# Optimization experiments

Measured on AMD Instinct MI355X. Metric: run time of the kernel, lower is better.

The kernel has to match this reference:

```python
import jax, jax.numpy as jnp
import numpy as np

B, N_ROIS, C, H, W = 4, 180, 512, 48, 48
STRIDE = 4
EPS = 1e-5


def _pool_one(feat, roi):
    # feat: [C,H,W], roi: [4] float (y1,x1,y2,x2) in image coords
    r = roi / STRIDE
    r0 = jnp.trunc(r[0]).astype(jnp.int32)
    r1 = jnp.trunc(r[1]).astype(jnp.int32)
    r2 = jnp.ceil(r[2]).astype(jnp.int32)
    r3 = jnp.ceil(r[3]).astype(jnp.int32)
    h_size = r2 - r0 + 1
    w_size = r3 - r1 + 1
    idx2 = jnp.arange(2)
    # AdaptiveMaxPool2d region boundaries: [floor(i*s/2), ceil((i+1)*s/2))
    sh = (idx2 * h_size) // 2
    eh = ((idx2 + 1) * h_size + 1) // 2
    sw = (idx2 * w_size) // 2
    ew = ((idx2 + 1) * w_size + 1) // 2
    hh = jnp.arange(H)[None, :]
    ww = jnp.arange(W)[None, :]
    mask_h = (hh >= (r0 + sh)[:, None]) & (hh < (r0 + eh)[:, None])  # [2,H]
    mask_w = (ww >= (r1 + sw)[:, None]) & (ww < (r1 + ew)[:, None])  # [2,W]
    neg = jnp.finfo(feat.dtype).min
    # max over W within each col region -> [2(oj), C, H]
    mw = jnp.where(mask_w[:, None, None, :], feat[None], neg).max(axis=-1)
    # max over H within each row region -> [2(oi), 2(oj), C]
    p = jnp.where(mask_h[:, None, None, :], mw[None], neg).max(axis=-1)
    # torch layout: [C, oi, oj] then flatten row-major
    return jnp.transpose(p, (2, 0, 1)).reshape(-1)  # [C*4]


def _roi_pool(features, rois):
    # features: [B,C,H,W], rois: [B,N,4] -> [B,N,C*4]
    def per_roi(roi_b):  # roi_b: [B,4]
        return jax.vmap(_pool_one)(features, roi_b)  # [B, C*4]
    out = jax.lax.map(per_roi, jnp.swapaxes(rois, 0, 1))  # [N,B,C*4]
    return jnp.swapaxes(out, 0, 1)


def _bn(x, gamma, beta):
    # training-mode BatchNorm1d over [B, N_ROIS(channels), F]: stats over (B,F)
    mean = x.mean(axis=(0, 2), keepdims=True)
    var = ((x - mean) ** 2).mean(axis=(0, 2), keepdims=True)
    return (x - mean) * jax.lax.rsqrt(var + EPS) * gamma[None, :, None] + beta[None, :, None]


def setup_inputs() -> dict:
    key = jax.random.key(0)
    k1, k2, k3, k4, k5 = jax.random.split(key, 5)
    features = jax.random.normal(k1, (B, C, H, W), dtype=jnp.float32)
    max_coord = (H - 1) * STRIDE
    y = jnp.sort(jax.random.uniform(k2, (B, N_ROIS, 2), minval=0.0, maxval=max_coord), axis=-1)
    x = jnp.sort(jax.random.uniform(k3, (B, N_ROIS, 2), minval=0.0, maxval=max_coord), axis=-1)
    rois = jnp.stack([y[..., 0], x[..., 0], y[..., 1], x[..., 1]], axis=-1)  # [B,N,4]
    F_in = C * 4
    W1 = jax.random.normal(k4, (64, F_in), dtype=jnp.float32) * 0.02
    bl1 = jnp.zeros((64,), dtype=jnp.float32)
    gamma1 = jnp.ones((N_ROIS,), dtype=jnp.float32)
    beta1 = jnp.zeros((N_ROIS,), dtype=jnp.float32)
    gamma2 = jnp.ones((N_ROIS,), dtype=jnp.float32)
    beta2 = jnp.zeros((N_ROIS,), dtype=jnp.float32)
    return {"features": features, "rois": rois, "gamma1": gamma1, "beta1": beta1,
            "W1": W1, "bl1": bl1, "gamma2": gamma2, "beta2": beta2}


def reference(features, rois, gamma1, beta1, W1, bl1, gamma2, beta2):
    pooled = _roi_pool(features, rois)            # [B, 180, 2048]
    x = jax.nn.relu(pooled)
    x = _bn(x, gamma1, beta1)
    y = jnp.einsum('bnf,of->bno', x, W1) + bl1    # [B, 180, 64]
    y = _bn(y, gamma2, beta2)
    return y
```

## Files before the change

### kernel.cpp

```cpp
#include <hip/hip_runtime.h>
#include <hip/hip_bf16.h>
#include <cfloat>
#include <math.h>

#define BB 4
#define NR 180
#define CC 512
#define HH 48
#define WW 48
#define FF (CC*4)
#define OO 64
#define EPSV 1e-5f
#define NCH 4


__device__ __forceinline__ void unpk(unsigned u, float& lo, float& hi) {
    lo = __uint_as_float(u << 16);
    hi = __uint_as_float(u & 0xffff0000u);
}
__device__ __forceinline__ unsigned pk(float lo, float hi) {
    return (__float_as_uint(lo) >> 16) | (__float_as_uint(hi) & 0xffff0000u);
}
__device__ __forceinline__ void acc8(float* cm, uint4 u) {
    float a, b;
    unpk(u.x, a, b); cm[0] = fmaxf(cm[0], a); cm[1] = fmaxf(cm[1], b);
    unpk(u.y, a, b); cm[2] = fmaxf(cm[2], a); cm[3] = fmaxf(cm[3], b);
    unpk(u.z, a, b); cm[4] = fmaxf(cm[4], a); cm[5] = fmaxf(cm[5], b);
    unpk(u.w, a, b); cm[6] = fmaxf(cm[6], a); cm[7] = fmaxf(cm[7], b);
}

__global__ __launch_bounds__(256) void k_prep(const float* __restrict__ feat,
                                              const float* __restrict__ W1,
                                              __hip_bfloat16* __restrict__ featB,
                                              float* __restrict__ W1T4) {
    __shared__ float tile[32][33];
    int t = threadIdx.x;
    int z = blockIdx.z;

    if (z < 4) {
        const int S = HH * WW;
        int b  = z;
        int s0 = blockIdx.x * 32;
        int c0 = blockIdx.y * 32;
        const float* src = feat + (size_t)b * CC * S;
        ushort* dst = (ushort*)featB + (size_t)b * S * CC;

        int cl = t >> 3;
        int sx = (t & 7) << 2;
        float4 v = *(const float4*)(src + (size_t)(c0 + cl) * S + s0 + sx);
        tile[cl][sx] = v.x; tile[cl][sx+1] = v.y; tile[cl][sx+2] = v.z; tile[cl][sx+3] = v.w;
        __syncthreads();

        int sl = t >> 3;
        int c4 = (t & 7) << 2;
        unsigned u0 = pk(tile[c4][sl],   tile[c4+1][sl]);
        unsigned u1 = pk(tile[c4+2][sl], tile[c4+3][sl]);
        *(uint2*)(dst + (size_t)(s0 + sl) * CC + c0 + c4) = make_uint2(u0, u1);
    } else {
        if (blockIdx.x >= 8) return;
        int kt = blockIdx.y * 8 + blockIdx.x;
        int k0 = (kt >> 1) * 32, o0 = (kt & 1) * 32;
        int tx = t & 31, ty = t >> 5;
        #pragma unroll
        for (int k = 0; k < 4; k++) {
            int row = ty + k * 8;
            tile[row][tx] = W1[(size_t)(o0 + row) * FF + (k0 + tx)];
        }
        __syncthreads();
        #pragma unroll
        for (int k = 0; k < 4; k++) {
            int row = ty + k * 8;
            int kk = k0 + row;
            int o  = o0 + tx;
            W1T4[(size_t)(kk >> 2) * 256 + o * 4 + (kk & 3)] = tile[tx][row];
        }
    }
}

__global__ __launch_bounds__(256, 6) void k_pool(const ushort* __restrict__ featB,
                                                 const float* __restrict__ rois,
                                                 ushort* __restrict__ pp) {
    __shared__ unsigned lu[4][16][64];
    int ch = blockIdx.x;
    int bn = blockIdx.y;
    int b = bn & 3, n = bn >> 2;
    int tid = threadIdx.x;
    int g  = tid >> 6;
    int c  = tid & 63;
    int c8 = c << 3;

    const float* roi = rois + ((size_t)b * NR + n) * 4;
    int r0 = (int)(roi[0] * 0.25f);
    int r1 = (int)(roi[1] * 0.25f);
    int r2 = (int)ceilf(roi[2] * 0.25f);
    int r3 = (int)ceilf(roi[3] * 0.25f);
    int hs  = r2 - r0 + 1;
    int wsz = r3 - r1 + 1;
    int eh0 = (hs + 1) >> 1, sh1 = hs >> 1;
    int ew0 = (wsz + 1) >> 1, sw1 = wsz >> 1;

    const float NEG = -FLT_MAX;
    float q00[8], q01[8], q10[8], q11[8];
    #pragma unroll
    for (int j = 0; j < 8; j++) { q00[j]=NEG; q01[j]=NEG; q10[j]=NEG; q11[j]=NEG; }

    for (int L = ch * 4 + g; L < hs; L += 16) {
        const ushort* rp = featB + ((size_t)((b * HH + r0 + L) * WW + r1)) * CC + c8;
        float cm0[8], cm1[8];
        #pragma unroll
        for (int j = 0; j < 8; j++) { cm0[j]=NEG; cm1[j]=NEG; }

        int w = 0;
        for (; w + 4 <= ew0; w += 4) {
            const ushort* p = rp + (size_t)w * CC;
            uint4 u0 = *(const uint4*)(p);
            uint4 u1 = *(const uint4*)(p + CC);
            uint4 u2 = *(const uint4*)(p + 2 * CC);
            uint4 u3 = *(const uint4*)(p + 3 * CC);
            acc8(cm0, u0); acc8(cm0, u1); acc8(cm0, u2); acc8(cm0, u3);
        }
        for (; w < ew0; w++) acc8(cm0, *(const uint4*)(rp + (size_t)w * CC));

        w = sw1;
        for (; w + 4 <= wsz; w += 4) {
            const ushort* p = rp + (size_t)w * CC;
            uint4 u0 = *(const uint4*)(p);
            uint4 u1 = *(const uint4*)(p + CC);
            uint4 u2 = *(const uint4*)(p + 2 * CC);
            uint4 u3 = *(const uint4*)(p + 3 * CC);
            acc8(cm1, u0); acc8(cm1, u1); acc8(cm1, u2); acc8(cm1, u3);
        }
        for (; w < wsz; w++) acc8(cm1, *(const uint4*)(rp + (size_t)w * CC));

        if (L < eh0) {
            #pragma unroll
            for (int j = 0; j < 8; j++) { q00[j]=fmaxf(q00[j],cm0[j]); q01[j]=fmaxf(q01[j],cm1[j]); }
        }
        if (L >= sh1) {
            #pragma unroll
            for (int j = 0; j < 8; j++) { q10[j]=fmaxf(q10[j],cm0[j]); q11[j]=fmaxf(q11[j],cm1[j]); }
        }
    }

    #pragma unroll
    for (int jc = 0; jc < 8; jc++) {
        lu[g][jc * 2 + 0][c] = pk(q00[jc], q01[jc]);
        lu[g][jc * 2 + 1][c] = pk(q10[jc], q11[jc]);
    }
    __syncthreads();

    int c2 = tid & 63, j0 = (tid >> 6) * 4;
    unsigned ou[4];
    #pragma unroll
    for (int jj = 0; jj < 4; jj++) {
        int j = j0 + jj;
        float lo = NEG, hi = NEG;
        #pragma unroll
        for (int gg = 0; gg < 4; gg++) {
            float a, bb2; unpk(lu[gg][j][c2], a, bb2);
            lo = fmaxf(lo, a); hi = fmaxf(hi, bb2);
        }
        lo = fmaxf(lo, 0.f); hi = fmaxf(hi, 0.f);
        ou[jj] = pk(lo, hi);
    }
    unsigned* dst = (unsigned*)(pp + ((size_t)(b * NR + n) * NCH + ch) * FF);
    *(uint4*)(dst + c2 * 16 + j0) = make_uint4(ou[0], ou[1], ou[2], ou[3]);
}

__global__ __launch_bounds__(1024) void k_gemm(const ushort* __restrict__ pp,
                                               const float* __restrict__ W1T4,
                                               const float* __restrict__ bl1,
                                               const float* __restrict__ g1,
                                               const float* __restrict__ b1,
                                               const float* __restrict__ g2,
                                               const float* __restrict__ b2,
                                               float* __restrict__ out) {
    __shared__ float xs[BB][FF];
    __shared__ float pd[16][BB][OO];
    __shared__ float pw[16][OO];
    __shared__ float part_s[16], part_q[16];
    __shared__ float sm2[4], sq2[4];
    int n = blockIdx.x;
    int tid = threadIdx.x;

    float s_acc = 0.f, q_acc = 0.f;
    #pragma unroll
    for (int k2 = 0; k2 < 2; k2++) {
        int gi = tid + (k2 << 10);
        int bb = gi >> 9;
        int idx = gi & 511;
        const unsigned* base = (const unsigned*)(pp + ((size_t)(bb * NR + n)) * NCH * FF);
        float v0 = -FLT_MAX, v1 = -FLT_MAX, v2 = -FLT_MAX, v3 = -FLT_MAX;
        #pragma unroll
        for (int cch = 0; cch < NCH; cch++) {
            uint2 u = *(const uint2*)(base + cch * (FF / 2) + idx * 2);
            float a, b_;
            unpk(u.x, a, b_); v0 = fmaxf(v0, a); v1 = fmaxf(v1, b_);
            unpk(u.y, a, b_); v2 = fmaxf(v2, a); v3 = fmaxf(v3, b_);
        }
        v0 = fmaxf(v0, 0.f); v1 = fmaxf(v1, 0.f); v2 = fmaxf(v2, 0.f); v3 = fmaxf(v3, 0.f);
        *(float4*)&xs[bb][idx << 2] = make_float4(v0, v1, v2, v3);
        s_acc += v0 + v1 + v2 + v3;
        q_acc += v0*v0 + v1*v1 + v2*v2 + v3*v3;
    }
    for (int off = 32; off; off >>= 1) {
        s_acc += __shfl_down(s_acc, off);
        q_acc += __shfl_down(q_acc, off);
    }
    if ((tid & 63) == 0) { part_s[tid >> 6] = s_acc; part_q[tid >> 6] = q_acc; }
    __syncthreads();
    float ts = 0.f, tq = 0.f;
    #pragma unroll
    for (int i = 0; i < 16; i++) { ts += part_s[i]; tq += part_q[i]; }
    const float inv1 = 1.f / (float)(BB * FF);
    float mean = ts * inv1;
    float var  = tq * inv1 - mean * mean;
    float a1n  = g1[n] * rsqrtf(var + EPSV);
    float c1n  = b1[n] - mean * a1n;

    int sc = tid >> 6;
    int o  = tid & 63;
    int k4a = sc << 5;
    float a0 = 0.f, a1 = 0.f, a2 = 0.f, a3 = 0.f, wsum = 0.f;
    #pragma unroll 4
    for (int k4 = k4a; k4 < k4a + 32; k4++) {
        float4 w4 = *(const float4*)(W1T4 + (size_t)k4 * 256 + o * 4);
        float4 x0 = *(const float4*)&xs[0][k4 << 2];
        float4 x1 = *(const float4*)&xs[1][k4 << 2];
        float4 x2 = *(const float4*)&xs[2][k4 << 2];
        float4 x3 = *(const float4*)&xs[3][k4 << 2];
        wsum += w4.x + w4.y + w4.z + w4.w;
        a0 += w4.x*x0.x + w4.y*x0.y + w4.z*x0.z + w4.w*x0.w;
        a1 += w4.x*x1.x + w4.y*x1.y + w4.z*x1.z + w4.w*x1.w;
        a2 += w4.x*x2.x + w4.y*x2.y + w4.z*x2.z + w4.w*x2.w;
        a3 += w4.x*x3.x + w4.y*x3.y + w4.z*x3.z + w4.w*x3.w;
    }
    pd[sc][0][o] = a0; pd[sc][1][o] = a1; pd[sc][2][o] = a2; pd[sc][3][o] = a3;
    pw[sc][o] = wsum;
    __syncthreads();

    float y = 0.f;
    int b = tid >> 6;
    if (tid < 256) {
        float dot = 0.f, wsm = 0.f;
        #pragma unroll
        for (int ss = 0; ss < 16; ss++) { dot += pd[ss][b][o]; wsm += pw[ss][o]; }
        y = a1n * dot + c1n * wsm + bl1[o];
        float rs = y, rq = y * y;
        for (int off = 32; off; off >>= 1) {
            rs += __shfl_down(rs, off);
            rq += __shfl_down(rq, off);
        }
        if (o == 0) { sm2[b] = rs; sq2[b] = rq; }
    }
    __syncthreads();
    if (tid < 256) {
        float sm  = sm2[0] + sm2[1] + sm2[2] + sm2[3];
        float sqm = sq2[0] + sq2[1] + sq2[2] + sq2[3];
        const float inv2 = 1.f / 256.f;
        float mean2 = sm * inv2;
        float var2  = sqm * inv2 - mean2 * mean2;
        float r2s = rsqrtf(var2 + EPSV);
        out[((size_t)b * NR + n) * OO + o] = (y - mean2) * r2s * g2[n] + b2[n];
    }
}

extern "C" void kernel_launch(void* const* d_in, const int* in_sizes, int n_in,
                              void* d_out, int out_size, void* d_ws, size_t ws_size,
                              hipStream_t stream) {
    const float* feat = (const float*)d_in[0];
    const float* rois = (const float*)d_in[1];
    const float* g1   = (const float*)d_in[2];
    const float* b1   = (const float*)d_in[3];
    const float* W1   = (const float*)d_in[4];
    const float* bl1  = (const float*)d_in[5];
    const float* g2   = (const float*)d_in[6];
    const float* b2   = (const float*)d_in[7];
    float* out = (float*)d_out;

    ushort* featB = (ushort*)d_ws;
    float*  W1T4  = (float*)(featB + (size_t)BB*HH*WW*CC);
    ushort* pp    = (ushort*)(W1T4 + (size_t)OO*FF);

    k_prep<<<dim3(72, 16, 5), 256, 0, stream>>>(feat, W1, (__hip_bfloat16*)featB, W1T4);
    k_pool<<<dim3(NCH, BB * NR), 256, 0, stream>>>(featB, rois, pp);
    k_gemm<<<NR, 1024, 0, stream>>>(pp, W1T4, bl1, g1, b1, g2, b2, out);
}
```

Before: 122.2 us.

## Encode bf16 features as order-preserving unsigned keys and use packed integer max

```diff
diff --git a/kernel.cpp b/kernel.cpp
--- a/kernel.cpp
+++ b/kernel.cpp
@@ -14,24 +14,30 @@
 #define NCH 4
 
 
-__device__ __forceinline__ void unpk(unsigned u, float& lo, float& hi) {
+typedef unsigned short us2 __attribute__((ext_vector_type(2)));
+
+__device__ __forceinline__ unsigned pmax(unsigned a, unsigned b) {
+    return __builtin_bit_cast(unsigned, __builtin_elementwise_max(
+        __builtin_bit_cast(us2, a), __builtin_bit_cast(us2, b)));
+}
+__device__ __forceinline__ uint4 pmax4(uint4 a, uint4 b) {
+    return make_uint4(pmax(a.x,b.x), pmax(a.y,b.y), pmax(a.z,b.z), pmax(a.w,b.w));
+}
+__device__ __forceinline__ unsigned mapb(float f) {
+    unsigned fu = __float_as_uint(f);
+    unsigned u = fu >> 16;
+    return (fu >> 31) ? (~u & 0xFFFFu) : (u | 0x8000u);
+}
+__device__ __forceinline__ void unmap2(unsigned m, float& lo, float& hi) {
+    unsigned t = ((~m) >> 15) & 0x00010001u;
+    unsigned u = m ^ (0x80008000u ^ (t * 0x7FFFu));
     lo = __uint_as_float(u << 16);
     hi = __uint_as_float(u & 0xffff0000u);
 }
-__device__ __forceinline__ unsigned pk(float lo, float hi) {
-    return (__float_as_uint(lo) >> 16) | (__float_as_uint(hi) & 0xffff0000u);
-}
-__device__ __forceinline__ void acc8(float* cm, uint4 u) {
-    float a, b;
-    unpk(u.x, a, b); cm[0] = fmaxf(cm[0], a); cm[1] = fmaxf(cm[1], b);
-    unpk(u.y, a, b); cm[2] = fmaxf(cm[2], a); cm[3] = fmaxf(cm[3], b);
-    unpk(u.z, a, b); cm[4] = fmaxf(cm[4], a); cm[5] = fmaxf(cm[5], b);
-    unpk(u.w, a, b); cm[6] = fmaxf(cm[6], a); cm[7] = fmaxf(cm[7], b);
-}
 
 __global__ __launch_bounds__(256) void k_prep(const float* __restrict__ feat,
                                               const float* __restrict__ W1,
-                                              __hip_bfloat16* __restrict__ featB,
+                                              ushort* __restrict__ featB,
                                               float* __restrict__ W1T4) {
     __shared__ float tile[32][33];
     int t = threadIdx.x;
@@ -43,7 +49,7 @@
         int s0 = blockIdx.x * 32;
         int c0 = blockIdx.y * 32;
         const float* src = feat + (size_t)b * CC * S;
-        ushort* dst = (ushort*)featB + (size_t)b * S * CC;
+        ushort* dst = featB + (size_t)b * S * CC;
 
         int cl = t >> 3;
         int sx = (t & 7) << 2;
@@ -53,8 +59,8 @@
 
         int sl = t >> 3;
         int c4 = (t & 7) << 2;
-        unsigned u0 = pk(tile[c4][sl],   tile[c4+1][sl]);
-        unsigned u1 = pk(tile[c4+2][sl], tile[c4+3][sl]);
+        unsigned u0 = mapb(tile[c4][sl])   | (mapb(tile[c4+1][sl]) << 16);
+        unsigned u1 = mapb(tile[c4+2][sl]) | (mapb(tile[c4+3][sl]) << 16);
         *(uint2*)(dst + (size_t)(s0 + sl) * CC + c0 + c4) = make_uint2(u0, u1);
     } else {
         if (blockIdx.x >= 8) return;
@@ -85,9 +91,7 @@
     int bn = blockIdx.y;
     int b = bn & 3, n = bn >> 2;
     int tid = threadIdx.x;
-    int g  = tid >> 6;
-    int c  = tid & 63;
-    int c8 = c << 3;
+    int g = tid >> 6, c = tid & 63;
 
     const float* roi = rois + ((size_t)b * NR + n) * 4;
     int r0 = (int)(roi[0] * 0.25f);
@@ -99,53 +103,81 @@
     int eh0 = (hs + 1) >> 1, sh1 = hs >> 1;
     int ew0 = (wsz + 1) >> 1, sw1 = wsz >> 1;
 
-    const float NEG = -FLT_MAX;
-    float q00[8], q01[8], q10[8], q11[8];
-    #pragma unroll
-    for (int j = 0; j < 8; j++) { q00[j]=NEG; q01[j]=NEG; q10[j]=NEG; q11[j]=NEG; }
+    const uint4 Z = make_uint4(0,0,0,0);
+    uint4 q00 = Z, q01 = Z, q10 = Z, q11 = Z;
 
     for (int L = ch * 4 + g; L < hs; L += 16) {
-        const ushort* rp = featB + ((size_t)((b * HH + r0 + L) * WW + r1)) * CC + c8;
-        float cm0[8], cm1[8];
-        #pragma unroll
-        for (int j = 0; j < 8; j++) { cm0[j]=NEG; cm1[j]=NEG; }
-
-        int w = 0;
-        for (; w + 4 <= ew0; w += 4) {
-            const ushort* p = rp + (size_t)w * CC;
-            uint4 u0 = *(const uint4*)(p);
-            uint4 u1 = *(const uint4*)(p + CC);
-            uint4 u2 = *(const uint4*)(p + 2 * CC);
-            uint4 u3 = *(const uint4*)(p + 3 * CC);
-            acc8(cm0, u0); acc8(cm0, u1); acc8(cm0, u2); acc8(cm0, u3);
-        }
-        for (; w < ew0; w++) acc8(cm0, *(const uint4*)(rp + (size_t)w * CC));
-
-        w = sw1;
-        for (; w + 4 <= wsz; w += 4) {
-            const ushort* p = rp + (size_t)w * CC;
-            uint4 u0 = *(const uint4*)(p);
-            uint4 u1 = *(const uint4*)(p + CC);
-            uint4 u2 = *(const uint4*)(p + 2 * CC);
-            uint4 u3 = *(const uint4*)(p + 3 * CC);
-            acc8(cm1, u0); acc8(cm1, u1); acc8(cm1, u2); acc8(cm1, u3);
-        }
-        for (; w < wsz; w++) acc8(cm1, *(const uint4*)(rp + (size_t)w * CC));
-
-        if (L < eh0) {
-            #pragma unroll
-            for (int j = 0; j < 8; j++) { q00[j]=fmaxf(q00[j],cm0[j]); q01[j]=fmaxf(q01[j],cm1[j]); }
-        }
-        if (L >= sh1) {
-            #pragma unroll
-            for (int j = 0; j < 8; j++) { q10[j]=fmaxf(q10[j],cm0[j]); q11[j]=fmaxf(q11[j],cm1[j]); }
-        }
-    }
-
-    #pragma unroll
-    for (int jc = 0; jc < 8; jc++) {
-        lu[g][jc * 2 + 0][c] = pk(q00[jc], q01[jc]);
-        lu[g][jc * 2 + 1][c] = pk(q10[jc], q11[jc]);
+        const uint4* rp = (const uint4*)(featB + ((size_t)((b * HH + r0 + L) * WW + r1)) * CC) + c;
+        uint4 cm0 = Z, cm1 = Z;
+        {
+            int e = ew0 - 1;
+            for (int w = 0; w < ew0; w += 8) {
+                uint4 u0 = rp[(size_t)64 * w];
+                uint4 u1 = rp[(size_t)64 * min(w + 1, e)];
+                uint4 u2 = rp[(size_t)64 * min(w + 2, e)];
+                uint4 u3 = rp[(size_t)64 * min(w + 3, e)];
+                uint4 u4 = rp[(size_t)64 * min(w + 4, e)];
+                uint4 u5 = rp[(size_t)64 * min(w + 5, e)];
+                uint4 u6 = rp[(size_t)64 * min(w + 6, e)];
+                uint4 u7 = rp[(size_t)64 * min(w + 7, e)];
+                cm0 = pmax4(cm0, pmax4(pmax4(pmax4(u0,u1), pmax4(u2,u3)),
+                                       pmax4(pmax4(u4,u5), pmax4(u6,u7))));
+            }
+        }
+        {
+            int e = wsz - 1;
+            for (int w = sw1; w < wsz; w += 8) {
+                uint4 u0 = rp[(size_t)64 * w];
+                uint4 u1 = rp[(size_t)64 * min(w + 1, e)];
+                uint4 u2 = rp[(size_t)64 * min(w + 2, e)];
+                uint4 u3 = rp[(size_t)64 * min(w + 3, e)];
+                uint4 u4 = rp[(size_t)64 * min(w + 4, e)];
+                uint4 u5 = rp[(size_t)64 * min(w + 5, e)];
+                uint4 u6 = rp[(size_t)64 * min(w + 6, e)];
+                uint4 u7 = rp[(size_t)64 * min(w + 7, e)];
+                cm1 = pmax4(cm1, pmax4(pmax4(pmax4(u0,u1), pmax4(u2,u3)),
+                                       pmax4(pmax4(u4,u5), pmax4(u6,u7))));
+            }
+        }
+        if (L <  eh0) { q00 = pmax4(q00, cm0); q01 = pmax4(q01, cm1); }
+        if (L >= sh1) { q10 = pmax4(q10, cm0); q11 = pmax4(q11, cm1); }
+    }
+
+    {
+        unsigned* L0 = &lu[g][0][c];
+        #define REPK(mcomp, a, bq, jc0) \
+            L0[((jc0)*2+0)*64]   = ((a) & 0xFFFFu) | ((bq) << 16); \
+            L0[((jc0)*2+0+2)*64] = ((a) >> 16) | ((bq) & 0xFFFF0000u);
+        #define REPK2(mcomp) { \
+            unsigned a0 = q00.mcomp, a1 = q01.mcomp, b0 = q10.mcomp, b1 = q11.mcomp; \
+            int jeven = (2*(&q00.mcomp - &q00.x)); (void)jeven; }
+        #undef REPK
+        #undef REPK2
+        unsigned a, b2;
+        a = q00.x; b2 = q01.x;
+        lu[g][0*4 + 0][c] = (a & 0xFFFFu) | (b2 << 16);
+        lu[g][0*4 + 2][c] = (a >> 16)     | (b2 & 0xFFFF0000u);
+        a = q10.x; b2 = q11.x;
+        lu[g][0*4 + 1][c] = (a & 0xFFFFu) | (b2 << 16);
+        lu[g][0*4 + 3][c] = (a >> 16)     | (b2 & 0xFFFF0000u);
+        a = q00.y; b2 = q01.y;
+        lu[g][1*4 + 0][c] = (a & 0xFFFFu) | (b2 << 16);
+        lu[g][1*4 + 2][c] = (a >> 16)     | (b2 & 0xFFFF0000u);
+        a = q10.y; b2 = q11.y;
+        lu[g][1*4 + 1][c] = (a & 0xFFFFu) | (b2 << 16);
+        lu[g][1*4 + 3][c] = (a >> 16)     | (b2 & 0xFFFF0000u);
+        a = q00.z; b2 = q01.z;
+        lu[g][2*4 + 0][c] = (a & 0xFFFFu) | (b2 << 16);
+        lu[g][2*4 + 2][c] = (a >> 16)     | (b2 & 0xFFFF0000u);
+        a = q10.z; b2 = q11.z;
+        lu[g][2*4 + 1][c] = (a & 0xFFFFu) | (b2 << 16);
+        lu[g][2*4 + 3][c] = (a >> 16)     | (b2 & 0xFFFF0000u);
+        a = q00.w; b2 = q01.w;
+        lu[g][3*4 + 0][c] = (a & 0xFFFFu) | (b2 << 16);
+        lu[g][3*4 + 2][c] = (a >> 16)     | (b2 & 0xFFFF0000u);
+        a = q10.w; b2 = q11.w;
+        lu[g][3*4 + 1][c] = (a & 0xFFFFu) | (b2 << 16);
+        lu[g][3*4 + 3][c] = (a >> 16)     | (b2 & 0xFFFF0000u);
     }
     __syncthreads();
 
@@ -154,18 +186,14 @@
     #pragma unroll
     for (int jj = 0; jj < 4; jj++) {
         int j = j0 + jj;
-        float lo = NEG, hi = NEG;
-        #pragma unroll
-        for (int gg = 0; gg < 4; gg++) {
-            float a, bb2; unpk(lu[gg][j][c2], a, bb2);
-            lo = fmaxf(lo, a); hi = fmaxf(hi, bb2);
-        }
-        lo = fmaxf(lo, 0.f); hi = fmaxf(hi, 0.f);
-        ou[jj] = pk(lo, hi);
+        unsigned m = pmax(pmax(lu[0][j][c2], lu[1][j][c2]),
+                          pmax(lu[2][j][c2], lu[3][j][c2]));
+        ou[jj] = pmax(m, 0x80008000u);
     }
     unsigned* dst = (unsigned*)(pp + ((size_t)(b * NR + n) * NCH + ch) * FF);
     *(uint4*)(dst + c2 * 16 + j0) = make_uint4(ou[0], ou[1], ou[2], ou[3]);
 }
+
 
 __global__ __launch_bounds__(1024) void k_gemm(const ushort* __restrict__ pp,
                                                const float* __restrict__ W1T4,
@@ -190,15 +218,16 @@
         int bb = gi >> 9;
         int idx = gi & 511;
         const unsigned* base = (const unsigned*)(pp + ((size_t)(bb * NR + n)) * NCH * FF);
-        float v0 = -FLT_MAX, v1 = -FLT_MAX, v2 = -FLT_MAX, v3 = -FLT_MAX;
+        uint2 m = *(const uint2*)(base + 0 * (FF / 2) + idx * 2);
         #pragma unroll
-        for (int cch = 0; cch < NCH; cch++) {
+        for (int cch = 1; cch < NCH; cch++) {
             uint2 u = *(const uint2*)(base + cch * (FF / 2) + idx * 2);
-            float a, b_;
-            unpk(u.x, a, b_); v0 = fmaxf(v0, a); v1 = fmaxf(v1, b_);
-            unpk(u.y, a, b_); v2 = fmaxf(v2, a); v3 = fmaxf(v3, b_);
-        }
-        v0 = fmaxf(v0, 0.f); v1 = fmaxf(v1, 0.f); v2 = fmaxf(v2, 0.f); v3 = fmaxf(v3, 0.f);
+            m.x = pmax(m.x, u.x);
+            m.y = pmax(m.y, u.y);
+        }
+        float v0, v1, v2, v3;
+        unmap2(m.x, v0, v1);
+        unmap2(m.y, v2, v3);
         *(float4*)&xs[bb][idx << 2] = make_float4(v0, v1, v2, v3);
         s_acc += v0 + v1 + v2 + v3;
         q_acc += v0*v0 + v1*v1 + v2*v2 + v3*v3;
@@ -282,7 +311,7 @@
     float*  W1T4  = (float*)(featB + (size_t)BB*HH*WW*CC);
     ushort* pp    = (ushort*)(W1T4 + (size_t)OO*FF);
 
-    k_prep<<<dim3(72, 16, 5), 256, 0, stream>>>(feat, W1, (__hip_bfloat16*)featB, W1T4);
+    k_prep<<<dim3(72, 16, 5), 256, 0, stream>>>(feat, W1, featB, W1T4);
     k_pool<<<dim3(NCH, BB * NR), 256, 0, stream>>>(featB, rois, pp);
     k_gemm<<<NR, 1024, 0, stream>>>(pp, W1T4, bl1, g1, b1, g2, b2, out);
 }
```

After: 117.4 us. 4.0% less time.
